# Performance work log

Measured on AMD Instinct MI355X. Metric: run time of the kernel, lower is better.

The kernel has to match this reference:

```python
import jax, jax.numpy as jnp
import numpy as np

N = 50000
IN_CH = 256
HID = 256
E = 800000


def setup_inputs() -> dict:
    key = jax.random.key(0)
    ks = jax.random.split(key, 12)
    s = 1.0 / np.sqrt(HID)
    return {
        "x": jax.random.normal(ks[0], (N, IN_CH), jnp.float32),
        "edge_index": jax.random.randint(ks[1], (2, E), 0, N, dtype=jnp.int64),
        "prev_embedding": jax.random.normal(ks[2], (N, HID), jnp.float32),
        "W1": jax.random.normal(ks[3], (IN_CH, HID), jnp.float32) / np.sqrt(IN_CH),
        "b1": jnp.zeros((HID,), jnp.float32),
        "W2": jax.random.normal(ks[4], (HID, HID), jnp.float32) * s,
        "b2": jnp.zeros((HID,), jnp.float32),
        "gWw": jax.random.normal(ks[5], (HID, HID), jnp.float32) * s,
        "gWb": jnp.zeros((HID,), jnp.float32),
        "gUw": jax.random.normal(ks[6], (HID, HID), jnp.float32) * s,
        "gUb": jnp.zeros((HID,), jnp.float32),
    }


def _gcn_conv(x, W, b, src, dst, norm):
    # PyG GCNConv: h = x @ W; out[i] = sum_j norm_ij * h[j]; + bias
    h = x @ W
    msg = h[src] * norm[:, None]  # [E+N, H]
    out = jax.ops.segment_sum(msg, dst, num_segments=N)
    return out + b


def _norm_and_loops(edge_index):
    loop = jnp.arange(N, dtype=edge_index.dtype)
    src = jnp.concatenate([edge_index[0], loop])
    dst = jnp.concatenate([edge_index[1], loop])
    deg = jax.ops.segment_sum(jnp.ones_like(dst, dtype=jnp.float32), dst, num_segments=N)
    dinv = jnp.where(deg > 0, jax.lax.rsqrt(deg), 0.0)
    norm = dinv[src] * dinv[dst]
    return src, dst, norm


def reference(x, edge_index, prev_embedding, W1, b1, W2, b2, gWw, gWb, gUw, gUb):
    src, dst, norm = _norm_and_loops(edge_index)
    h = jax.nn.relu(_gcn_conv(x, W1, b1, src, dst, norm))
    h_t = _gcn_conv(h, W2, b2, src, dst, norm)
    alpha = jax.nn.sigmoid(h_t @ gWw + gWb + prev_embedding @ gUw + gUb)
    h_tilde = alpha * h_t + (1.0 - alpha) * prev_embedding
    return (h_tilde, h_t)
```

## Files before the change

kernel.cpp:

```cpp
#include <hip/hip_runtime.h>
#include <hip/hip_bf16.h>
#include <math.h>

#define HIDC 256
#define LSTR 56

typedef short short8 __attribute__((ext_vector_type(8)));
typedef float f32x4 __attribute__((ext_vector_type(4)));

__device__ __forceinline__ ushort f2bf_rne(float f) {
    uint u = __float_as_uint(f);
    u += 0x7FFF + ((u >> 16) & 1);
    return (ushort)(u >> 16);
}
__device__ __forceinline__ float bf2f(ushort h) {
    return __uint_as_float(((uint)h) << 16);
}


__global__ void fill_i_kernel(int* __restrict__ p, int v, int n) {
    int i = blockIdx.x * 256 + threadIdx.x;
    if (i < n) p[i] = v;
}

__global__ void deg_kernel(const int* __restrict__ dst, int* __restrict__ deg, int E) {
    int e = blockIdx.x * 256 + threadIdx.x;
    if (e < E) atomicAdd(&deg[dst[e]], 1);
}

__global__ void rsqrt_kernel(const int* __restrict__ deg, float* __restrict__ dinv, int n) {
    int i = blockIdx.x * 256 + threadIdx.x;
    if (i < n) dinv[i] = rsqrtf((float)(deg[i] + 1));
}


__device__ __forceinline__ int block_incl_scan(int v, int tid) {
#pragma unroll
    for (int off = 1; off < 64; off <<= 1) {
        int t = __shfl_up(v, off);
        if ((tid & 63) >= off) v += t;
    }
    __shared__ int wt[4];
    if ((tid & 63) == 63) wt[tid >> 6] = v;
    __syncthreads();
    int wid = tid >> 6;
    for (int w = 0; w < wid; w++) v += wt[w];
    __syncthreads();
    return v;
}

__global__ void scan_a_kernel(const int* __restrict__ deg, int* __restrict__ row_start,
                              int* __restrict__ blocksum, int N) {
    int tid = threadIdx.x;
    int i = blockIdx.x * 256 + tid;
    int v = (i < N) ? deg[i] : 0;
    int incl = block_incl_scan(v, tid);
    if (i < N) row_start[i + 1] = incl;
    if (tid == 255) blocksum[blockIdx.x] = incl;
}

__global__ void scan_b_kernel(int* __restrict__ blocksum, int nb) {
    int tid = threadIdx.x;
    int v = (tid < nb) ? blocksum[tid] : 0;
    int incl = block_incl_scan(v, tid);
    if (tid < nb) blocksum[tid] = incl;
}

__global__ void scan_c_kernel(int* __restrict__ row_start, int* __restrict__ cursor,
                              const int* __restrict__ blocksum, int N) {
    int b = blockIdx.x;
    int i = b * 256 + threadIdx.x;
    int add = (b > 0) ? blocksum[b - 1] : 0;
    if (i < N) {
        int v = row_start[i + 1] + add;
        row_start[i + 1] = v;
        cursor[i + 1] = v;
    }
    if (b == 0 && threadIdx.x == 0) { row_start[0] = 0; cursor[0] = 0; }
}

__global__ void scatter_kernel(const int* __restrict__ src, const int* __restrict__ dst,
                               const float* __restrict__ dinv, int* __restrict__ cursor,
                               int* __restrict__ csr_src, float* __restrict__ csr_w, int E) {
    int e = blockIdx.x * 256 + threadIdx.x;
    if (e < E) {
        int s = src[e], d = dst[e];
        int pos = atomicAdd(&cursor[d], 1);
        csr_src[pos] = s;
        csr_w[pos] = dinv[s] * dinv[d];
    }
}


__global__ void prep_bt_kernel(const float* __restrict__ B, ushort* __restrict__ Bt) {
    int n = blockIdx.x, k = threadIdx.x;
    Bt[n * 256 + k] = f2bf_rne(B[k * 256 + n]);
}

__global__ void prep_gate_bt_kernel(const float* __restrict__ gWw, const float* __restrict__ gUw,
                                    ushort* __restrict__ Bth, ushort* __restrict__ Btl) {
    int n = blockIdx.x, k = threadIdx.x;
    float v1 = gWw[k * 256 + n];
    uint u1 = __float_as_uint(v1);
    Bth[n * 512 + k] = (ushort)(u1 >> 16);
    Btl[n * 512 + k] = f2bf_rne(v1 - __uint_as_float(u1 & 0xFFFF0000u));
    float v2 = gUw[k * 256 + n];
    uint u2 = __float_as_uint(v2);
    Bth[n * 512 + 256 + k] = (ushort)(u2 >> 16);
    Btl[n * 512 + 256 + k] = f2bf_rne(v2 - __uint_as_float(u2 & 0xFFFF0000u));
}


__global__ __launch_bounds__(256) void gemm_bf16_kernel(
    const float* __restrict__ A, const ushort* __restrict__ Bt,
    ushort* __restrict__ C, int M)
{
    __shared__ __align__(16) ushort As[128 * LSTR];
    __shared__ __align__(16) ushort Bs[128 * LSTR];
    const int tl = threadIdx.x;
    const int lane = tl & 63, wave = tl >> 6;
    const int wm = (wave & 1) * 64, wn = (wave >> 1) * 64;
    const int bm = blockIdx.x * 128, bn = blockIdx.y * 128;

    const int ar  = tl >> 1;
    const int akq = (tl & 1) * 16;
    const bool aok = (bm + ar) < M;

    f32x4 acc[4][4] = {};

    for (int k0 = 0; k0 < 256; k0 += 32) {
        {
            const float* ap = A + (size_t)(bm + ar) * HIDC + k0 + akq;
#pragma unroll
            for (int j = 0; j < 4; j++) {
                float4 v = aok ? *(const float4*)(ap + 4 * j) : make_float4(0.f, 0.f, 0.f, 0.f);
                ushort4 h;
                h.x = f2bf_rne(v.x); h.y = f2bf_rne(v.y);
                h.z = f2bf_rne(v.z); h.w = f2bf_rne(v.w);
                *(ushort4*)&As[ar * LSTR + akq + 4 * j] = h;
            }
        }
        {
            const ushort* bp = Bt + (size_t)(bn + ar) * 256 + k0 + akq;
            *(uint4*)&Bs[ar * LSTR + akq]     = *(const uint4*)bp;
            *(uint4*)&Bs[ar * LSTR + akq + 8] = *(const uint4*)(bp + 8);
        }
        __syncthreads();
        const int fr = lane & 15, koff = (lane >> 4) * 8;
        short8 af[4], bfv[4];
#pragma unroll
        for (int t = 0; t < 4; t++) {
            af[t]  = *(const short8*)&As[(wm + t * 16 + fr) * LSTR + koff];
            bfv[t] = *(const short8*)&Bs[(wn + t * 16 + fr) * LSTR + koff];
        }
#pragma unroll
        for (int mt = 0; mt < 4; mt++)
#pragma unroll
            for (int nt = 0; nt < 4; nt++)
                acc[mt][nt] = __builtin_amdgcn_mfma_f32_16x16x32_bf16(af[mt], bfv[nt], acc[mt][nt], 0, 0, 0);
        __syncthreads();
    }

    const int row4 = (lane >> 4) * 4, coln = lane & 15;
#pragma unroll
    for (int mt = 0; mt < 4; mt++)
#pragma unroll
        for (int r = 0; r < 4; r++) {
            int m = bm + wm + mt * 16 + row4 + r;
            if (m < M) {
#pragma unroll
                for (int nt = 0; nt < 4; nt++) {
                    int n = bn + wn + nt * 16 + coln;
                    C[(size_t)m * HIDC + n] = f2bf_rne(acc[mt][nt][r]);
                }
            }
        }
}


__global__ __launch_bounds__(256) void gate_kernel(
    const float* __restrict__ ht, const float* __restrict__ prev,
    const ushort* __restrict__ Bth, const ushort* __restrict__ Btl,
    const float* __restrict__ gWb, const float* __restrict__ gUb,
    float* __restrict__ out, int M)
{
    __shared__ __align__(16) ushort Ash[128 * LSTR];
    __shared__ __align__(16) ushort Asl[128 * LSTR];
    __shared__ __align__(16) ushort Bsh[128 * LSTR];
    __shared__ __align__(16) ushort Bsl[128 * LSTR];
    const int tl = threadIdx.x;
    const int lane = tl & 63, wave = tl >> 6;
    const int wm = (wave & 1) * 64, wn = (wave >> 1) * 64;
    const int bm = blockIdx.x * 128, bn = blockIdx.y * 128;

    const int ar  = tl >> 1;
    const int akq = (tl & 1) * 16;
    const bool aok = (bm + ar) < M;

    f32x4 acc[4][4] = {};

    for (int k0 = 0; k0 < 512; k0 += 32) {
        {
            const float* srcA = (k0 < 256) ? ht : prev;
            const float* ap = srcA + (size_t)(bm + ar) * HIDC + (k0 & 255) + akq;
#pragma unroll
            for (int j = 0; j < 4; j++) {
                float4 v = aok ? *(const float4*)(ap + 4 * j) : make_float4(0.f, 0.f, 0.f, 0.f);
                float vv[4] = {v.x, v.y, v.z, v.w};
                ushort4 hh, ll;
                ushort* hp = (ushort*)&hh; ushort* lp = (ushort*)&ll;
#pragma unroll
                for (int q = 0; q < 4; q++) {
                    uint u = __float_as_uint(vv[q]);
                    hp[q] = (ushort)(u >> 16);
                    lp[q] = f2bf_rne(vv[q] - __uint_as_float(u & 0xFFFF0000u));
                }
                *(ushort4*)&Ash[ar * LSTR + akq + 4 * j] = hh;
                *(ushort4*)&Asl[ar * LSTR + akq + 4 * j] = ll;
            }
        }
        {
            const ushort* bph = Bth + (size_t)(bn + ar) * 512 + k0 + akq;
            const ushort* bpl = Btl + (size_t)(bn + ar) * 512 + k0 + akq;
            *(uint4*)&Bsh[ar * LSTR + akq]     = *(const uint4*)bph;
            *(uint4*)&Bsh[ar * LSTR + akq + 8] = *(const uint4*)(bph + 8);
            *(uint4*)&Bsl[ar * LSTR + akq]     = *(const uint4*)bpl;
            *(uint4*)&Bsl[ar * LSTR + akq + 8] = *(const uint4*)(bpl + 8);
        }
        __syncthreads();
        const int fr = lane & 15, koff = (lane >> 4) * 8;
        short8 afh[4], afl[4], bfh[4], bfl[4];
#pragma unroll
        for (int t = 0; t < 4; t++) {
            afh[t] = *(const short8*)&Ash[(wm + t * 16 + fr) * LSTR + koff];
            afl[t] = *(const short8*)&Asl[(wm + t * 16 + fr) * LSTR + koff];
            bfh[t] = *(const short8*)&Bsh[(wn + t * 16 + fr) * LSTR + koff];
            bfl[t] = *(const short8*)&Bsl[(wn + t * 16 + fr) * LSTR + koff];
        }
#pragma unroll
        for (int mt = 0; mt < 4; mt++)
#pragma unroll
            for (int nt = 0; nt < 4; nt++) {
                acc[mt][nt] = __builtin_amdgcn_mfma_f32_16x16x32_bf16(afh[mt], bfh[nt], acc[mt][nt], 0, 0, 0);
                acc[mt][nt] = __builtin_amdgcn_mfma_f32_16x16x32_bf16(afh[mt], bfl[nt], acc[mt][nt], 0, 0, 0);
                acc[mt][nt] = __builtin_amdgcn_mfma_f32_16x16x32_bf16(afl[mt], bfh[nt], acc[mt][nt], 0, 0, 0);
            }
        __syncthreads();
    }

    const int row4 = (lane >> 4) * 4, coln = lane & 15;
#pragma unroll
    for (int mt = 0; mt < 4; mt++)
#pragma unroll
        for (int r = 0; r < 4; r++) {
            int m = bm + wm + mt * 16 + row4 + r;
            if (m < M) {
#pragma unroll
                for (int nt = 0; nt < 4; nt++) {
                    int n = bn + wn + nt * 16 + coln;
                    size_t idx = (size_t)m * HIDC + n;
                    float g = acc[mt][nt][r] + gWb[n] + gUb[n];
                    float alpha = 1.f / (1.f + expf(-g));
                    out[idx] = alpha * ht[idx] + (1.f - alpha) * prev[idx];
                }
            }
        }
}


__global__ __launch_bounds__(256) void csr_agg_kernel(
    const ushort* __restrict__ hm, const int* __restrict__ row_start,
    const int* __restrict__ csr_src, const float* __restrict__ csr_w,
    const float* __restrict__ dinv, const float* __restrict__ bias,
    float* __restrict__ out, int do_relu) {
    __shared__ int   s_idx[64];
    __shared__ float s_w[64];
    const int i = blockIdx.x;
    const int c = threadIdx.x;
    const int b0 = row_start[i];
    const int b1 = row_start[i + 1];
    const float di = dinv[i];
    float acc = di * di * bf2f(hm[(size_t)i * HIDC + c]);
    for (int cb = b0; cb < b1; cb += 64) {
        int m = min(64, b1 - cb);
        if (c < m) {
            s_idx[c] = csr_src[cb + c];
            s_w[c]   = csr_w[cb + c];
        }
        __syncthreads();
        for (int t = 0; t < m; t++) {
            int s = s_idx[t];
            acc += s_w[t] * bf2f(hm[(size_t)s * HIDC + c]);
        }
        __syncthreads();
    }
    acc += bias[c];
    if (do_relu) acc = fmaxf(acc, 0.f);
    out[(size_t)i * HIDC + c] = acc;
}


extern "C" void kernel_launch(void* const* d_in, const int* in_sizes, int n_in,
                              void* d_out, int out_size, void* d_ws, size_t ws_size,
                              hipStream_t stream) {
    const float* x    = (const float*)d_in[0];
    const int*   ei   = (const int*)d_in[1];
    const float* prev = (const float*)d_in[2];
    const float* W1   = (const float*)d_in[3];
    const float* b1   = (const float*)d_in[4];
    const float* W2   = (const float*)d_in[5];
    const float* b2   = (const float*)d_in[6];
    const float* gWw  = (const float*)d_in[7];
    const float* gWb  = (const float*)d_in[8];
    const float* gUw  = (const float*)d_in[9];
    const float* gUb  = (const float*)d_in[10];

    const int N = in_sizes[0] / HIDC;
    const int E = in_sizes[1] / 2;
    const int* src = ei;
    const int* dst = ei + E;

    float* out  = (float*)d_out;
    float* out1 = out;
    float* ht   = out + (size_t)N * HIDC;

    float* ws = (float*)d_ws;
    size_t o = 0;
    auto take = [&](size_t n) { size_t r = o; o += (n + 63) & ~(size_t)63; return r; };
    float*  dinv    = ws + take(N);
    int*    degi    = (int*)(ws + take(N));
    int*    row_st  = (int*)(ws + take(N + 1));
    int*    cursor  = (int*)(ws + take(N + 1));
    int*    csr_src = (int*)(ws + take(E));
    float*  csr_w   = ws + take(E);
    ushort* Bt1     = (ushort*)(ws + take(256 * 256 / 2));
    ushort* Bt2     = (ushort*)(ws + take(256 * 256 / 2));
    ushort* Bth     = (ushort*)(ws + take(256 * 512 / 2));
    ushort* Btl     = (ushort*)(ws + take(256 * 512 / 2));
    ushort* hm      = (ushort*)(ws + take((size_t)N * HIDC / 2));

    const int nbN = (N + 255) / 256;
    const int nbE = (E + 255) / 256;
    dim3 ggrid((N + 127) / 128, 2);

    int* blocksum = (int*)csr_w;
    fill_i_kernel<<<nbN, 256, 0, stream>>>(degi, 0, N);
    deg_kernel<<<nbE, 256, 0, stream>>>(dst, degi, E);
    scan_a_kernel<<<nbN, 256, 0, stream>>>(degi, row_st, blocksum, N);
    scan_b_kernel<<<1, 256, 0, stream>>>(blocksum, nbN);
    scan_c_kernel<<<nbN, 256, 0, stream>>>(row_st, cursor, blocksum, N);
    rsqrt_kernel<<<nbN, 256, 0, stream>>>(degi, dinv, N);
    scatter_kernel<<<nbE, 256, 0, stream>>>(src, dst, dinv, cursor, csr_src, csr_w, E);

    prep_bt_kernel<<<256, 256, 0, stream>>>(W1, Bt1);
    prep_bt_kernel<<<256, 256, 0, stream>>>(W2, Bt2);
    prep_gate_bt_kernel<<<256, 256, 0, stream>>>(gWw, gUw, Bth, Btl);

    gemm_bf16_kernel<<<ggrid, 256, 0, stream>>>(x, Bt1, hm, N);
    csr_agg_kernel<<<N, 256, 0, stream>>>(hm, row_st, csr_src, csr_w, dinv, b1, out1, 1);

    gemm_bf16_kernel<<<ggrid, 256, 0, stream>>>(out1, Bt2, hm, N);
    csr_agg_kernel<<<N, 256, 0, stream>>>(hm, row_st, csr_src, csr_w, dinv, b2, ht, 0);

    gate_kernel<<<ggrid, 256, 0, stream>>>(ht, prev, Bth, Btl, gWb, gUb, out1, N);

    (void)n_in; (void)out_size; (void)ws_size;
}
```

Before: 608.5 us.

## Slice GEMM output by channel, pack CSR edges, and drop split-bf16 gate GEMM

Result: slower. 930.5 us (+52.9%).

```diff
diff --git a/kernel.cpp b/kernel.cpp
--- a/kernel.cpp
+++ b/kernel.cpp
@@ -81,13 +81,12 @@
 
 __global__ void scatter_kernel(const int* __restrict__ src, const int* __restrict__ dst,
                                const float* __restrict__ dinv, int* __restrict__ cursor,
-                               int* __restrict__ csr_src, float* __restrict__ csr_w, int E) {
+                               int2* __restrict__ csr_e, int E) {
     int e = blockIdx.x * 256 + threadIdx.x;
     if (e < E) {
         int s = src[e], d = dst[e];
         int pos = atomicAdd(&cursor[d], 1);
-        csr_src[pos] = s;
-        csr_w[pos] = dinv[s] * dinv[d];
+        csr_e[pos] = make_int2(s, __float_as_int(dinv[s] * dinv[d]));
     }
 }
 
@@ -98,16 +97,10 @@
 }
 
 __global__ void prep_gate_bt_kernel(const float* __restrict__ gWw, const float* __restrict__ gUw,
-                                    ushort* __restrict__ Bth, ushort* __restrict__ Btl) {
+                                    ushort* __restrict__ Bt) {
     int n = blockIdx.x, k = threadIdx.x;
-    float v1 = gWw[k * 256 + n];
-    uint u1 = __float_as_uint(v1);
-    Bth[n * 512 + k] = (ushort)(u1 >> 16);
-    Btl[n * 512 + k] = f2bf_rne(v1 - __uint_as_float(u1 & 0xFFFF0000u));
-    float v2 = gUw[k * 256 + n];
-    uint u2 = __float_as_uint(v2);
-    Bth[n * 512 + 256 + k] = (ushort)(u2 >> 16);
-    Btl[n * 512 + 256 + k] = f2bf_rne(v2 - __uint_as_float(u2 & 0xFFFF0000u));
+    Bt[n * 512 + k]       = f2bf_rne(gWw[k * 256 + n]);
+    Bt[n * 512 + 256 + k] = f2bf_rne(gUw[k * 256 + n]);
 }
 
 
@@ -162,6 +155,7 @@
     }
 
     const int row4 = (lane >> 4) * 4, coln = lane & 15;
+    const int Mn = M;
 #pragma unroll
     for (int mt = 0; mt < 4; mt++)
 #pragma unroll
@@ -171,7 +165,8 @@
 #pragma unroll
                 for (int nt = 0; nt < 4; nt++) {
                     int n = bn + wn + nt * 16 + coln;
-                    C[(size_t)m * HIDC + n] = f2bf_rne(acc[mt][nt][r]);
+                    C[(size_t)(n >> 5) * Mn * 32 + (size_t)m * 32 + (n & 31)] =
+                        f2bf_rne(acc[mt][nt][r]);
                 }
             }
         }
@@ -180,14 +175,12 @@
 
 __global__ __launch_bounds__(256) void gate_kernel(
     const float* __restrict__ ht, const float* __restrict__ prev,
-    const ushort* __restrict__ Bth, const ushort* __restrict__ Btl,
+    const ushort* __restrict__ Bt,
     const float* __restrict__ gWb, const float* __restrict__ gUb,
     float* __restrict__ out, int M)
 {
-    __shared__ __align__(16) ushort Ash[128 * LSTR];
-    __shared__ __align__(16) ushort Asl[128 * LSTR];
-    __shared__ __align__(16) ushort Bsh[128 * LSTR];
-    __shared__ __align__(16) ushort Bsl[128 * LSTR];
+    __shared__ __align__(16) ushort As[128 * LSTR];
+    __shared__ __align__(16) ushort Bs[128 * LSTR];
     const int tl = threadIdx.x;
     const int lane = tl & 63, wave = tl >> 6;
     const int wm = (wave & 1) * 64, wn = (wave >> 1) * 64;
@@ -206,45 +199,30 @@
 #pragma unroll
             for (int j = 0; j < 4; j++) {
                 float4 v = aok ? *(const float4*)(ap + 4 * j) : make_float4(0.f, 0.f, 0.f, 0.f);
-                float vv[4] = {v.x, v.y, v.z, v.w};
-                ushort4 hh, ll;
-                ushort* hp = (ushort*)&hh; ushort* lp = (ushort*)&ll;
-#pragma unroll
-                for (int q = 0; q < 4; q++) {
-                    uint u = __float_as_uint(vv[q]);
-                    hp[q] = (ushort)(u >> 16);
-                    lp[q] = f2bf_rne(vv[q] - __uint_as_float(u & 0xFFFF0000u));
-                }
-                *(ushort4*)&Ash[ar * LSTR + akq + 4 * j] = hh;
-                *(ushort4*)&Asl[ar * LSTR + akq + 4 * j] = ll;
+                ushort4 h;
+                h.x = f2bf_rne(v.x); h.y = f2bf_rne(v.y);
+                h.z = f2bf_rne(v.z); h.w = f2bf_rne(v.w);
+                *(ushort4*)&As[ar * LSTR + akq + 4 * j] = h;
             }
         }
         {
-            const ushort* bph = Bth + (size_t)(bn + ar) * 512 + k0 + akq;
-            const ushort* bpl = Btl + (size_t)(bn + ar) * 512 + k0 + akq;
-            *(uint4*)&Bsh[ar * LSTR + akq]     = *(const uint4*)bph;
-            *(uint4*)&Bsh[ar * LSTR + akq + 8] = *(const uint4*)(bph + 8);
-            *(uint4*)&Bsl[ar * LSTR + akq]     = *(const uint4*)bpl;
-            *(uint4*)&Bsl[ar * LSTR + akq + 8] = *(const uint4*)(bpl + 8);
+            const ushort* bp = Bt + (size_t)(bn + ar) * 512 + k0 + akq;
+            *(uint4*)&Bs[ar * LSTR + akq]     = *(const uint4*)bp;
+            *(uint4*)&Bs[ar * LSTR + akq + 8] = *(const uint4*)(bp + 8);
         }
         __syncthreads();
         const int fr = lane & 15, koff = (lane >> 4) * 8;
-        short8 afh[4], afl[4], bfh[4], bfl[4];
+        short8 af[4], bfv[4];
 #pragma unroll
         for (int t = 0; t < 4; t++) {
-            afh[t] = *(const short8*)&Ash[(wm + t * 16 + fr) * LSTR + koff];
-            afl[t] = *(const short8*)&Asl[(wm + t * 16 + fr) * LSTR + koff];
-            bfh[t] = *(const short8*)&Bsh[(wn + t * 16 + fr) * LSTR + koff];
-            bfl[t] = *(const short8*)&Bsl[(wn + t * 16 + fr) * LSTR + koff];
+            af[t]  = *(const short8*)&As[(wm + t * 16 + fr) * LSTR + koff];
+            bfv[t] = *(const short8*)&Bs[(wn + t * 16 + fr) * LSTR + koff];
         }
 #pragma unroll
         for (int mt = 0; mt < 4; mt++)
 #pragma unroll
-            for (int nt = 0; nt < 4; nt++) {
-                acc[mt][nt] = __builtin_amdgcn_mfma_f32_16x16x32_bf16(afh[mt], bfh[nt], acc[mt][nt], 0, 0, 0);
-                acc[mt][nt] = __builtin_amdgcn_mfma_f32_16x16x32_bf16(afh[mt], bfl[nt], acc[mt][nt], 0, 0, 0);
-                acc[mt][nt] = __builtin_amdgcn_mfma_f32_16x16x32_bf16(afl[mt], bfh[nt], acc[mt][nt], 0, 0, 0);
-            }
+            for (int nt = 0; nt < 4; nt++)
+                acc[mt][nt] = __builtin_amdgcn_mfma_f32_16x16x32_bf16(af[mt], bfv[nt], acc[mt][nt], 0, 0, 0);
         __syncthreads();
     }
 
@@ -268,35 +246,33 @@
 }
 
 
-__global__ __launch_bounds__(256) void csr_agg_kernel(
-    const ushort* __restrict__ hm, const int* __restrict__ row_start,
-    const int* __restrict__ csr_src, const float* __restrict__ csr_w,
-    const float* __restrict__ dinv, const float* __restrict__ bias,
-    float* __restrict__ out, int do_relu) {
-    __shared__ int   s_idx[64];
-    __shared__ float s_w[64];
-    const int i = blockIdx.x;
-    const int c = threadIdx.x;
-    const int b0 = row_start[i];
-    const int b1 = row_start[i + 1];
-    const float di = dinv[i];
-    float acc = di * di * bf2f(hm[(size_t)i * HIDC + c]);
-    for (int cb = b0; cb < b1; cb += 64) {
-        int m = min(64, b1 - cb);
-        if (c < m) {
-            s_idx[c] = csr_src[cb + c];
-            s_w[c]   = csr_w[cb + c];
-        }
-        __syncthreads();
-        for (int t = 0; t < m; t++) {
-            int s = s_idx[t];
-            acc += s_w[t] * bf2f(hm[(size_t)s * HIDC + c]);
-        }
-        __syncthreads();
-    }
-    acc += bias[c];
-    if (do_relu) acc = fmaxf(acc, 0.f);
-    out[(size_t)i * HIDC + c] = acc;
+__global__ __launch_bounds__(256) void csr_agg_sliced_kernel(
+    const ushort* __restrict__ hm_s, const int* __restrict__ row_start,
+    const int2* __restrict__ csr_e, const float* __restrict__ dinv,
+    const float* __restrict__ bias, float* __restrict__ out,
+    int N, int do_relu)
+{
+    const int slice = blockIdx.x;
+    const int node  = blockIdx.y * 4 + (threadIdx.x >> 6);
+    const int lane  = threadIdx.x & 63;
+    const int half  = lane >> 5;
+    const int c     = lane & 31;
+    if (node >= N) return;
+    const ushort* tab = hm_s + (size_t)slice * N * 32;
+    const int b0 = row_start[node], b1 = row_start[node + 1];
+    const float di = dinv[node];
+    float acc = half ? 0.f : di * di * bf2f(tab[(size_t)node * 32 + c]);
+    for (int j = b0 + half; j < b1; j += 2) {
+        int2 e = csr_e[j];
+        acc += __int_as_float(e.y) * bf2f(tab[(size_t)e.x * 32 + c]);
+    }
+    acc += __shfl(acc, lane ^ 32);
+    if (!half) {
+        int ch = slice * 32 + c;
+        float v = acc + bias[ch];
+        if (do_relu) v = fmaxf(v, 0.f);
+        out[(size_t)node * HIDC + ch] = v;
+    }
 }
 
 
@@ -331,38 +307,37 @@
     int*    degi    = (int*)(ws + take(N));
     int*    row_st  = (int*)(ws + take(N + 1));
     int*    cursor  = (int*)(ws + take(N + 1));
-    int*    csr_src = (int*)(ws + take(E));
-    float*  csr_w   = ws + take(E);
+    int2*   csr_e   = (int2*)(ws + take(2 * (size_t)E));
     ushort* Bt1     = (ushort*)(ws + take(256 * 256 / 2));
     ushort* Bt2     = (ushort*)(ws + take(256 * 256 / 2));
-    ushort* Bth     = (ushort*)(ws + take(256 * 512 / 2));
-    ushort* Btl     = (ushort*)(ws + take(256 * 512 / 2));
+    ushort* Btg     = (ushort*)(ws + take(256 * 512 / 2));
     ushort* hm      = (ushort*)(ws + take((size_t)N * HIDC / 2));
 
     const int nbN = (N + 255) / 256;
     const int nbE = (E + 255) / 256;
     dim3 ggrid((N + 127) / 128, 2);
-
-    int* blocksum = (int*)csr_w;
+    dim3 agrid(8, (N + 3) / 4);
+
+    int* blocksum = (int*)csr_e;
     fill_i_kernel<<<nbN, 256, 0, stream>>>(degi, 0, N);
     deg_kernel<<<nbE, 256, 0, stream>>>(dst, degi, E);
     scan_a_kernel<<<nbN, 256, 0, stream>>>(degi, row_st, blocksum, N);
     scan_b_kernel<<<1, 256, 0, stream>>>(blocksum, nbN);
     scan_c_kernel<<<nbN, 256, 0, stream>>>(row_st, cursor, blocksum, N);
     rsqrt_kernel<<<nbN, 256, 0, stream>>>(degi, dinv, N);
-    scatter_kernel<<<nbE, 256, 0, stream>>>(src, dst, dinv, cursor, csr_src, csr_w, E);
+    scatter_kernel<<<nbE, 256, 0, stream>>>(src, dst, dinv, cursor, csr_e, E);
 
     prep_bt_kernel<<<256, 256, 0, stream>>>(W1, Bt1);
     prep_bt_kernel<<<256, 256, 0, stream>>>(W2, Bt2);
-    prep_gate_bt_kernel<<<256, 256, 0, stream>>>(gWw, gUw, Bth, Btl);
+    prep_gate_bt_kernel<<<256, 256, 0, stream>>>(gWw, gUw, Btg);
 
     gemm_bf16_kernel<<<ggrid, 256, 0, stream>>>(x, Bt1, hm, N);
-    csr_agg_kernel<<<N, 256, 0, stream>>>(hm, row_st, csr_src, csr_w, dinv, b1, out1, 1);
+    csr_agg_sliced_kernel<<<agrid, 256, 0, stream>>>(hm, row_st, csr_e, dinv, b1, out1, N, 1);
 
     gemm_bf16_kernel<<<ggrid, 256, 0, stream>>>(out1, Bt2, hm, N);
-    csr_agg_kernel<<<N, 256, 0, stream>>>(hm, row_st, csr_src, csr_w, dinv, b2, ht, 0);
-
-    gate_kernel<<<ggrid, 256, 0, stream>>>(ht, prev, Bth, Btl, gWb, gUb, out1, N);
+    csr_agg_sliced_kernel<<<agrid, 256, 0, stream>>>(hm, row_st, csr_e, dinv, b2, ht, N, 0);
+
+    gate_kernel<<<ggrid, 256, 0, stream>>>(ht, prev, Btg, gWb, gUb, out1, N);
 
     (void)n_in; (void)out_size; (void)ws_size;
 }
```
